# Performance work log

Hardware: AMD Instinct MI355X
Metric: run time of the kernel (lower is better)

## Reference

```python
import jax, jax.numpy as jnp
import numpy as np

# Standard bitsandbytes NF4 codebook (16 values)
NF4_CODE = jnp.array([
    -1.0, -0.6961928009986877, -0.5250730514526367, -0.39491748809814453,
    -0.28444138169288635, -0.18477343022823334, -0.09105003625154495, 0.0,
    0.07958029955625534, 0.16093020141124725, 0.24611230194568634,
    0.33791524171829224, 0.44070982933044434, 0.5626170039176941,
    0.7229568362236023, 1.0], dtype=jnp.float32)

BLOCKSIZE = 64
IN_FEATURES = 4096
OUT_FEATURES = 11008


def setup_inputs() -> dict:
    key = jax.random.key(0)
    k1, k2, k3, k4 = jax.random.split(key, 4)
    x = jax.random.normal(k1, (4, 2048, IN_FEATURES), dtype=jnp.float32)
    weight_q = jax.random.randint(k2, (OUT_FEATURES, IN_FEATURES), 0, 16, dtype=jnp.int32)
    absmax = jax.random.uniform(k3, (OUT_FEATURES, IN_FEATURES // BLOCKSIZE), dtype=jnp.float32)
    bias = jax.random.normal(k4, (OUT_FEATURES,), dtype=jnp.float32)
    return {"x": x, "weight_q": weight_q, "absmax": absmax, "bias": bias}


def reference(x, weight_q, absmax, bias):
    out_f, in_f = weight_q.shape
    # Blockwise NF4 dequantization: code lookup * per-block absmax scale
    w_code = NF4_CODE[weight_q]                                   # [O, I]
    w_blocks = w_code.reshape(out_f, in_f // BLOCKSIZE, BLOCKSIZE)
    w = (w_blocks * absmax[:, :, None]).reshape(out_f, in_f)      # [O, I]
    # Linear: y = x @ W^T + b
    y = jnp.einsum('bsi,oi->bso', x, w) + bias
    return y
```

## Files before the change

kernel.cpp:

```cpp
#include <hip/hip_runtime.h>
#include <hip/hip_bf16.h>
#include <stdint.h>

typedef __attribute__((ext_vector_type(8))) short short8;
typedef __attribute__((ext_vector_type(8))) unsigned short ushort8;
typedef __attribute__((ext_vector_type(4))) float f32x4;

#define K_DIM 4096
#define N_DIM 11008
#define M_DIM 8192
#define BM 256
#define BN 256
#define BK 64
#define TILES (K_DIM / BK)

__constant__ float c_nf4[16] = {
    -1.0f, -0.6961928009986877f, -0.5250730514526367f, -0.39491748809814453f,
    -0.28444138169288635f, -0.18477343022823334f, -0.09105003625154495f, 0.0f,
    0.07958029955625534f, 0.16093020141124725f, 0.24611230194568634f,
    0.33791524171829224f, 0.44070982933044434f, 0.5626170039176941f,
    0.7229568362236023f, 1.0f};

__device__ __forceinline__ unsigned short f2bf(float f) {
    uint32_t u = __float_as_uint(f);
    u += 0x7fffu + ((u >> 16) & 1u);
    return (unsigned short)(u >> 16);
}

__global__ __launch_bounds__(256) void nf4_dequant_w(const int* __restrict__ q,
                                                     const float* __restrict__ absmax,
                                                     unsigned short* __restrict__ w) {
    __shared__ float lut[16];
    if (threadIdx.x < 16) lut[threadIdx.x] = c_nf4[threadIdx.x];
    __syncthreads();
    size_t t = (size_t)blockIdx.x * 256 + threadIdx.x;
    const int4* q4 = (const int4*)q;
    int4 qa = q4[2 * t];
    int4 qb = q4[2 * t + 1];
    float s = absmax[t >> 3];
    ushort8 o;
    o[0] = f2bf(lut[qa.x & 15] * s);
    o[1] = f2bf(lut[qa.y & 15] * s);
    o[2] = f2bf(lut[qa.z & 15] * s);
    o[3] = f2bf(lut[qa.w & 15] * s);
    o[4] = f2bf(lut[qb.x & 15] * s);
    o[5] = f2bf(lut[qb.y & 15] * s);
    o[6] = f2bf(lut[qb.z & 15] * s);
    o[7] = f2bf(lut[qb.w & 15] * s);
    ((ushort8*)w)[t] = o;
}

__global__ __launch_bounds__(256) void x_to_bf16(const float* __restrict__ x,
                                                 unsigned short* __restrict__ xb) {
    size_t t = (size_t)blockIdx.x * 256 + threadIdx.x;
    const float4* x4 = (const float4*)x;
    float4 a = x4[2 * t];
    float4 b = x4[2 * t + 1];
    ushort8 o;
    o[0] = f2bf(a.x); o[1] = f2bf(a.y); o[2] = f2bf(a.z); o[3] = f2bf(a.w);
    o[4] = f2bf(b.x); o[5] = f2bf(b.y); o[6] = f2bf(b.z); o[7] = f2bf(b.w);
    ((ushort8*)xb)[t] = o;
}

#define STAGE_HALF(gbase, lds_half, row0, k0)                                 \
  do {                                                                        \
    _Pragma("unroll")                                                         \
    for (int _g = 0; _g < 2; ++_g) {                                          \
      const int _i = _g * 512 + tid;                        \
      const int _r = _i >> 3;                           \
      const int _c = (_i & 7) ^ (_r & 7);                   \
      __builtin_amdgcn_global_load_lds(                                       \
          (const __attribute__((address_space(1))) void*)((gbase) +           \
              (size_t)((row0) + _r) * K_DIM + (k0) + _c * 8),                 \
          (__attribute__((address_space(3))) void*)((lds_half) +              \
              (_g * 512 + wave * 64) * 8),                                    \
          16, 0, 0);                                                          \
    }                                                                         \
  } while (0)

#define DS_A4(dst, rbase, X)                                                  \
  dst[0] = *(const short8*)(Ah + ((rbase) +  0) * 64 + (roff ^ (X)));         \
  dst[1] = *(const short8*)(Ah + ((rbase) + 16) * 64 + (roff ^ (X)));         \
  dst[2] = *(const short8*)(Ah + ((rbase) + 32) * 64 + (roff ^ (X)));         \
  dst[3] = *(const short8*)(Ah + ((rbase) + 48) * 64 + (roff ^ (X)));

#define DS_B4(dst, X)                                                         \
  dst[0] = *(const short8*)(Bh + (bbase +  0) * 64 + (roff ^ (X)));           \
  dst[1] = *(const short8*)(Bh + (bbase + 16) * 64 + (roff ^ (X)));           \
  dst[2] = *(const short8*)(Bh + (bbase + 32) * 64 + (roff ^ (X)));           \
  dst[3] = *(const short8*)(Bh + (bbase + 48) * 64 + (roff ^ (X)));

#define MFMA16(MI0, Ar, Br)                                                   \
  do {                                                                        \
    _Pragma("unroll")                                                         \
    for (int _m = 0; _m < 4; ++_m) {                                          \
      _Pragma("unroll")                                                       \
      for (int _n = 0; _n < 4; ++_n)                                          \
        acc[(MI0) + _m][_n] = __builtin_amdgcn_mfma_f32_16x16x32_bf16(        \
            Ar[_m], Br[_n], acc[(MI0) + _m][_n], 0, 0, 0);                    \
    }                                                                         \
  } while (0)

#define BAR   asm volatile("s_barrier" ::: "memory")
#define LGKM0 do { asm volatile("s_waitcnt lgkmcnt(0)" ::: "memory");         \
                   __builtin_amdgcn_sched_barrier(0); } while (0)

#define PHASE_MFMA(MI0, Ar, Br)                                               \
  BAR; LGKM0;                                                                 \
  __builtin_amdgcn_s_setprio(1);                                              \
  MFMA16(MI0, Ar, Br);                                                        \
  __builtin_amdgcn_s_setprio(0);                                              \
  __builtin_amdgcn_sched_barrier(0)

__global__ __launch_bounds__(512, 2) void gemm256(const unsigned short* __restrict__ A,
                                                  const unsigned short* __restrict__ B,
                                                  const float* __restrict__ bias,
                                                  float* __restrict__ C) {
    __shared__ unsigned short As[2][2][128 * 64];
    __shared__ unsigned short Bs[2][2][128 * 64];

    const int tid  = threadIdx.x;
    const int wave = tid >> 6;
    const int lane = tid & 63;
    const int wm = wave >> 2;
    const int wn = wave & 3;
    const int lr = lane & 15;
    const int q  = lane >> 4;
    const int roff = lr * 64 + ((q ^ (lr & 7)) << 3);
    const int bbase = (wn & 1) * 64;

    const int nbn = N_DIM / BN;
    const int cpx = (int)gridDim.x >> 3;
    const int bid = (int)blockIdx.x;
    const int swz = (bid & 7) * cpx + (bid >> 3);
    const int bm = swz / nbn;
    const int bn = swz % nbn;

    const unsigned short* Ab = A + (size_t)bm * BM * K_DIM;
    const unsigned short* Bb = B + (size_t)bn * BN * K_DIM;

    f32x4 acc[8][4];
#pragma unroll
    for (int i = 0; i < 8; ++i)
#pragma unroll
        for (int j = 0; j < 4; ++j)
#pragma unroll
            for (int v = 0; v < 4; ++v) acc[i][j][v] = 0.0f;

    STAGE_HALF(Ab, &As[0][0][0], 0,   0); STAGE_HALF(Bb, &Bs[0][0][0], 0,   0);
    STAGE_HALF(Ab, &As[0][1][0], 128, 0); STAGE_HALF(Bb, &Bs[0][1][0], 128, 0);
    asm volatile("s_waitcnt vmcnt(0)" ::: "memory");
    BAR;

    short8 aA[4], aB[4], aC[4], aD[4], bE[4], bO[4];

#pragma unroll 1
    for (int t = 0; t < TILES; ++t) {
        const int p = t & 1;
        int t1 = t + 1; if (t1 >= TILES) t1 = 0;
        const int k1 = t1 * BK;
        const unsigned short* Ah = &As[p][wm][0];
        const unsigned short* Bh = &Bs[p][wn >> 1][0];

        DS_A4(aA, 0, 0);
        DS_B4(bE, 0);
        STAGE_HALF(Ab, &As[p ^ 1][0][0], 0, k1);
        STAGE_HALF(Bb, &Bs[p ^ 1][0][0], 0, k1);
        PHASE_MFMA(0, aA, bE);
        BAR;

        DS_A4(aB, 64, 0);
        STAGE_HALF(Ab, &As[p ^ 1][1][0], 128, k1);
        PHASE_MFMA(4, aB, bE);
        BAR;

        DS_A4(aC, 0, 32);
        DS_B4(bO, 32);
        STAGE_HALF(Bb, &Bs[p ^ 1][1][0], 128, k1);
        PHASE_MFMA(0, aC, bO);
        BAR;

        DS_A4(aD, 64, 32);
        PHASE_MFMA(4, aD, bO);
        asm volatile("s_waitcnt vmcnt(0)" ::: "memory");
        BAR;
    }
    asm volatile("s_waitcnt vmcnt(0)" ::: "memory");

    const int row0 = bm * BM + wm * 128 + (q << 2);
    const int col0 = bn * BN + wn * 64 + lr;
#pragma unroll
    for (int ni = 0; ni < 4; ++ni) {
        const int col = col0 + ni * 16;
        const float bv = bias[col];
#pragma unroll
        for (int mi = 0; mi < 8; ++mi) {
#pragma unroll
            for (int v = 0; v < 4; ++v) {
                C[(size_t)(row0 + mi * 16 + v) * N_DIM + col] = acc[mi][ni][v] + bv;
            }
        }
    }
}

extern "C" void kernel_launch(void* const* d_in, const int* in_sizes, int n_in,
                              void* d_out, int out_size, void* d_ws, size_t ws_size,
                              hipStream_t stream) {
    const float* x    = (const float*)d_in[0];
    const int*   wq   = (const int*)d_in[1];
    const float* am   = (const float*)d_in[2];
    const float* bias = (const float*)d_in[3];
    float* out = (float*)d_out;

    const size_t w_elems = (size_t)N_DIM * K_DIM;
    const size_t x_elems = (size_t)M_DIM * K_DIM;
    const size_t need = (w_elems + x_elems) * sizeof(unsigned short);
    if (ws_size < need) return;

    unsigned short* wbf = (unsigned short*)d_ws;
    unsigned short* xbf = wbf + w_elems;

    nf4_dequant_w<<<(int)(w_elems / 8 / 256), 256, 0, stream>>>(wq, am, wbf);
    x_to_bf16<<<(int)(x_elems / 8 / 256), 256, 0, stream>>>(x, xbf);

    const int grid = (M_DIM / BM) * (N_DIM / BN);
    gemm256<<<grid, 512, 0, stream>>>(xbf, wbf, bias, out);
}
```

Before: 975.6 us.

## Unroll GEMM main loop by two tiles with deeper cross-tile prefetch and quadrant MFMA phases

Restructures the bf16 GEMM main loop to handle two K tiles per iteration. The prologue now preloads almost two full tiles, and global-to-LDS staging for tile t+2/t+3 is spread across eight compute phases, with partial vmcnt waits replacing full drains. Each phase now computes an M×N quadrant over both K halves, which lets A fragments be reused across two phases instead of being reloaded. The aim is to keep more loads in flight and hide latency better. The cost is more register pressure and a more delicate barrier and waitcnt ordering that could race or spill.

```diff
diff --git a/kernel.cpp b/kernel.cpp
--- a/kernel.cpp
+++ b/kernel.cpp
@@ -13,6 +13,7 @@
 #define BN 256
 #define BK 64
 #define TILES (K_DIM / BK)
+#define ITERS (TILES / 2)
 
 __constant__ float c_nf4[16] = {
     -1.0f, -0.6961928009986877f, -0.5250730514526367f, -0.39491748809814453f,
@@ -66,9 +67,9 @@
   do {                                                                        \
     _Pragma("unroll")                                                         \
     for (int _g = 0; _g < 2; ++_g) {                                          \
-      const int _i = _g * 512 + tid;                        \
-      const int _r = _i >> 3;                           \
-      const int _c = (_i & 7) ^ (_r & 7);                   \
+      const int _i = _g * 512 + tid;                                          \
+      const int _r = _i >> 3;                                                 \
+      const int _c = (_i & 7) ^ (_r & 7);                                     \
       __builtin_amdgcn_global_load_lds(                                       \
           (const __attribute__((address_space(1))) void*)((gbase) +           \
               (size_t)((row0) + _r) * K_DIM + (k0) + _c * 8),                 \
@@ -78,39 +79,48 @@
     }                                                                         \
   } while (0)
 
-#define DS_A4(dst, rbase, X)                                                  \
-  dst[0] = *(const short8*)(Ah + ((rbase) +  0) * 64 + (roff ^ (X)));         \
-  dst[1] = *(const short8*)(Ah + ((rbase) + 16) * 64 + (roff ^ (X)));         \
-  dst[2] = *(const short8*)(Ah + ((rbase) + 32) * 64 + (roff ^ (X)));         \
-  dst[3] = *(const short8*)(Ah + ((rbase) + 48) * 64 + (roff ^ (X)));
-
-#define DS_B4(dst, X)                                                         \
-  dst[0] = *(const short8*)(Bh + (bbase +  0) * 64 + (roff ^ (X)));           \
-  dst[1] = *(const short8*)(Bh + (bbase + 16) * 64 + (roff ^ (X)));           \
-  dst[2] = *(const short8*)(Bh + (bbase + 32) * 64 + (roff ^ (X)));           \
-  dst[3] = *(const short8*)(Bh + (bbase + 48) * 64 + (roff ^ (X)));
-
-#define MFMA16(MI0, Ar, Br)                                                   \
+#define DS_A8(dst, Ah, qr)                                                    \
   do {                                                                        \
     _Pragma("unroll")                                                         \
     for (int _m = 0; _m < 4; ++_m) {                                          \
+      dst[_m][0] = *(const short8*)((Ah) + ((qr) + _m * 16) * 64 + roff);     \
+      dst[_m][1] = *(const short8*)((Ah) + ((qr) + _m * 16) * 64 + (roff ^ 32)); \
+    }                                                                         \
+  } while (0)
+
+#define DS_B4(dst, Bh, qc)                                                    \
+  do {                                                                        \
+    _Pragma("unroll")                                                         \
+    for (int _n = 0; _n < 2; ++_n) {                                          \
+      dst[_n][0] = *(const short8*)((Bh) + (lb + (qc) + _n * 16) * 64 + roff); \
+      dst[_n][1] = *(const short8*)((Bh) + (lb + (qc) + _n * 16) * 64 + (roff ^ 32)); \
+    }                                                                         \
+  } while (0)
+
+#define MFMAQ(MI0, NI0, Ar, Br)                                               \
+  do {                                                                        \
+    _Pragma("unroll")                                                         \
+    for (int _k = 0; _k < 2; ++_k) {                                          \
       _Pragma("unroll")                                                       \
-      for (int _n = 0; _n < 4; ++_n)                                          \
-        acc[(MI0) + _m][_n] = __builtin_amdgcn_mfma_f32_16x16x32_bf16(        \
-            Ar[_m], Br[_n], acc[(MI0) + _m][_n], 0, 0, 0);                    \
+      for (int _m = 0; _m < 4; ++_m) {                                        \
+        _Pragma("unroll")                                                     \
+        for (int _n = 0; _n < 2; ++_n)                                        \
+          acc[(MI0) + _m][(NI0) + _n] = __builtin_amdgcn_mfma_f32_16x16x32_bf16( \
+              Ar[_m][_k], Br[_n][_k], acc[(MI0) + _m][(NI0) + _n], 0, 0, 0);  \
+      }                                                                       \
     }                                                                         \
   } while (0)
 
 #define BAR   asm volatile("s_barrier" ::: "memory")
-#define LGKM0 do { asm volatile("s_waitcnt lgkmcnt(0)" ::: "memory");         \
-                   __builtin_amdgcn_sched_barrier(0); } while (0)
-
-#define PHASE_MFMA(MI0, Ar, Br)                                               \
+#define SB0   __builtin_amdgcn_sched_barrier(0)
+#define LGKM0 do { asm volatile("s_waitcnt lgkmcnt(0)" ::: "memory"); SB0; } while (0)
+
+#define PH_COMPUTE(MI0, NI0, Ar, Br)                                          \
   BAR; LGKM0;                                                                 \
   __builtin_amdgcn_s_setprio(1);                                              \
-  MFMA16(MI0, Ar, Br);                                                        \
+  MFMAQ(MI0, NI0, Ar, Br);                                                    \
   __builtin_amdgcn_s_setprio(0);                                              \
-  __builtin_amdgcn_sched_barrier(0)
+  SB0;
 
 __global__ __launch_bounds__(512, 2) void gemm256(const unsigned short* __restrict__ A,
                                                   const unsigned short* __restrict__ B,
@@ -127,7 +137,7 @@
     const int lr = lane & 15;
     const int q  = lane >> 4;
     const int roff = lr * 64 + ((q ^ (lr & 7)) << 3);
-    const int bbase = (wn & 1) * 64;
+    const int lb = (wn & 1) * 64;
 
     const int nbn = N_DIM / BN;
     const int cpx = (int)gridDim.x >> 3;
@@ -147,42 +157,77 @@
 #pragma unroll
             for (int v = 0; v < 4; ++v) acc[i][j][v] = 0.0f;
 
-    STAGE_HALF(Ab, &As[0][0][0], 0,   0); STAGE_HALF(Bb, &Bs[0][0][0], 0,   0);
-    STAGE_HALF(Ab, &As[0][1][0], 128, 0); STAGE_HALF(Bb, &Bs[0][1][0], 128, 0);
-    asm volatile("s_waitcnt vmcnt(0)" ::: "memory");
+    STAGE_HALF(Bb, &Bs[0][0][0], 0,   0);
+    STAGE_HALF(Bb, &Bs[0][1][0], 128, 0);
+    STAGE_HALF(Ab, &As[0][0][0], 0,   0);
+    STAGE_HALF(Ab, &As[0][1][0], 128, 0);
+    STAGE_HALF(Bb, &Bs[1][0][0], 0,   BK);
+    STAGE_HALF(Bb, &Bs[1][1][0], 128, BK);
+    STAGE_HALF(Ab, &As[1][0][0], 0,   BK);
+    asm volatile("s_waitcnt vmcnt(6)" ::: "memory");
     BAR;
 
-    short8 aA[4], aB[4], aC[4], aD[4], bE[4], bO[4];
+    short8 aS[4][2], aT[4][2], b0[2][2], b1[2][2];
 
 #pragma unroll 1
-    for (int t = 0; t < TILES; ++t) {
-        const int p = t & 1;
-        int t1 = t + 1; if (t1 >= TILES) t1 = 0;
-        const int k1 = t1 * BK;
-        const unsigned short* Ah = &As[p][wm][0];
-        const unsigned short* Bh = &Bs[p][wn >> 1][0];
-
-        DS_A4(aA, 0, 0);
-        DS_B4(bE, 0);
-        STAGE_HALF(Ab, &As[p ^ 1][0][0], 0, k1);
-        STAGE_HALF(Bb, &Bs[p ^ 1][0][0], 0, k1);
-        PHASE_MFMA(0, aA, bE);
-        BAR;
-
-        DS_A4(aB, 64, 0);
-        STAGE_HALF(Ab, &As[p ^ 1][1][0], 128, k1);
-        PHASE_MFMA(4, aB, bE);
-        BAR;
-
-        DS_A4(aC, 0, 32);
-        DS_B4(bO, 32);
-        STAGE_HALF(Bb, &Bs[p ^ 1][1][0], 128, k1);
-        PHASE_MFMA(0, aC, bO);
-        BAR;
-
-        DS_A4(aD, 64, 32);
-        PHASE_MFMA(4, aD, bO);
-        asm volatile("s_waitcnt vmcnt(0)" ::: "memory");
+    for (int i = 0; i < ITERS; ++i) {
+        const int u  = 2 * i;
+        const int v  = (u + 1) & (TILES - 1);
+        const int t2 = (u + 2) & (TILES - 1);
+        const int t3 = (u + 3) & (TILES - 1);
+        const unsigned short* A0 = &As[0][wm][0];
+        const unsigned short* B0h = &Bs[0][wn >> 1][0];
+        const unsigned short* A1 = &As[1][wm][0];
+        const unsigned short* B1h = &Bs[1][wn >> 1][0];
+
+        DS_A8(aS, A0, 0);
+        DS_B4(b0, B0h, 0);
+        STAGE_HALF(Ab, &As[1][1][0], 128, v * BK);
+        PH_COMPUTE(0, 0, aS, b0);
+        BAR;
+
+        DS_B4(b1, B0h, 32);
+        PH_COMPUTE(0, 2, aS, b1);
+        BAR;
+
+        DS_A8(aT, A0, 64);
+        STAGE_HALF(Bb, &Bs[0][0][0], 0, t2 * BK);
+        PH_COMPUTE(4, 0, aT, b0);
+        BAR;
+
+        STAGE_HALF(Bb, &Bs[0][1][0], 128, t2 * BK);
+        BAR; SB0;
+        __builtin_amdgcn_s_setprio(1);
+        MFMAQ(4, 2, aT, b1);
+        __builtin_amdgcn_s_setprio(0);
+        SB0;
+        asm volatile("s_waitcnt vmcnt(4)" ::: "memory");
+        BAR;
+
+        DS_A8(aS, A1, 0);
+        DS_B4(b0, B1h, 0);
+        STAGE_HALF(Ab, &As[0][0][0], 0, t2 * BK);
+        PH_COMPUTE(0, 0, aS, b0);
+        BAR;
+
+        DS_B4(b1, B1h, 32);
+        STAGE_HALF(Ab, &As[0][1][0], 128, t2 * BK);
+        PH_COMPUTE(0, 2, aS, b1);
+        BAR;
+
+        DS_A8(aT, A1, 64);
+        STAGE_HALF(Bb, &Bs[1][0][0], 0, t3 * BK);
+        PH_COMPUTE(4, 0, aT, b0);
+        BAR;
+
+        STAGE_HALF(Bb, &Bs[1][1][0], 128, t3 * BK);
+        STAGE_HALF(Ab, &As[1][0][0], 0, t3 * BK);
+        BAR; SB0;
+        __builtin_amdgcn_s_setprio(1);
+        MFMAQ(4, 2, aT, b1);
+        __builtin_amdgcn_s_setprio(0);
+        SB0;
+        asm volatile("s_waitcnt vmcnt(6)" ::: "memory");
         BAR;
     }
     asm volatile("s_waitcnt vmcnt(0)" ::: "memory");
@@ -196,8 +241,8 @@
 #pragma unroll
         for (int mi = 0; mi < 8; ++mi) {
 #pragma unroll
-            for (int v = 0; v < 4; ++v) {
-                C[(size_t)(row0 + mi * 16 + v) * N_DIM + col] = acc[mi][ni][v] + bv;
+            for (int vv = 0; vv < 4; ++vv) {
+                C[(size_t)(row0 + mi * 16 + vv) * N_DIM + col] = acc[mi][ni][vv] + bv;
             }
         }
     }
```

New measurement: 861.8 us. 1.13x faster.
